# Optimization experiments

Measured on AMD Instinct MI355X. Metric: run time of the kernel, lower is better.

Reference implementation:

```python
import jax, jax.numpy as jnp
import numpy as np

VOCAB, EMBED, HIDDEN, NCLS = 32000, 512, 1024, 1000
BATCH, SEQ = 128, 512


def setup_inputs() -> dict:
    key = jax.random.key(0)
    ks = jax.random.split(key, 8)
    s_in = 1.0 / np.sqrt(EMBED + HIDDEN)
    s_h = 1.0 / np.sqrt(HIDDEN)
    return {
        "x": jax.random.randint(ks[0], (BATCH, SEQ), 0, VOCAB, dtype=jnp.int32),
        "emb": jax.random.normal(ks[1], (VOCAB, EMBED), dtype=jnp.float32),
        "Wz": jax.random.uniform(ks[2], (EMBED + HIDDEN, HIDDEN), jnp.float32, -s_in, s_in),
        "bz": jax.random.uniform(ks[3], (HIDDEN,), jnp.float32, -s_in, s_in),
        "Wh": jax.random.uniform(ks[4], (EMBED + HIDDEN, HIDDEN), jnp.float32, -s_in, s_in),
        "bh": jax.random.uniform(ks[5], (HIDDEN,), jnp.float32, -s_in, s_in),
        "Wfc": jax.random.uniform(ks[6], (HIDDEN, NCLS), jnp.float32, -s_h, s_h),
        "bfc": jax.random.uniform(ks[7], (NCLS,), jnp.float32, -s_h, s_h),
    }


def reference(x, emb, Wz, bz, Wh, bh, Wfc, bfc):
    # embedding lookup: [B, S, E]
    e = emb[x]
    B = x.shape[0]
    h0 = jnp.zeros((B, Wz.shape[1]), dtype=emb.dtype)

    def step(h, x_t):
        c = jnp.concatenate([x_t, h], axis=1)          # [B, E+H]
        z = jax.nn.sigmoid(c @ Wz + bz)                # forget/update gate
        h_tilde = jnp.tanh(c @ Wh + bh)                # candidate state
        h_new = (1.0 - z) * h + z * h_tilde
        return h_new, None

    h_final, _ = jax.lax.scan(step, h0, jnp.swapaxes(e, 0, 1))  # scan over S
    return h_final @ Wfc + bfc                          # logits [B, NCLS]
```

## Files before the change

### kernel.cpp

```cpp
#include <hip/hip_runtime.h>

#define BATCH 128
#define SEQ   512
#define EMB   512
#define HID   1024
#define KC    1536
#define NCLS  1000
#define NBLK  128
#define TPB   512

using short8 = __attribute__((ext_vector_type(8))) short;
using f32x4  = __attribute__((ext_vector_type(4))) float;
typedef unsigned long long u64;

__device__ __forceinline__ short f2bf(float f) {
    unsigned u = __float_as_uint(f);
    unsigned r = (u + 0x7fffu + ((u >> 16) & 1u)) >> 16;
    return (short)r;
}
__device__ __forceinline__ float bf2f(short s) {
    unsigned u = ((unsigned)(unsigned short)s) << 16;
    return __uint_as_float(u);
}

#define OFF_CH0 0u
#define OFF_CL0 262144u
#define OFF_BAR 524288u
#define OFF_CH1 526336u
#define OFF_CL1 788480u
#define OFF_H   1050624u
#define ZERO_I4 32896u

__global__ void mgu_init(int4* __restrict__ ws4) {
    unsigned i = blockIdx.x * blockDim.x + threadIdx.x;
    if (i < ZERO_I4) ws4[i] = make_int4(0, 0, 0, 0);
}

__global__ __launch_bounds__(TPB, 1) void mgu_scan(
    const int* __restrict__ x, const float* __restrict__ emb,
    const float* __restrict__ Wz, const float* __restrict__ bz,
    const float* __restrict__ Wh, const float* __restrict__ bh,
    short* __restrict__ ch0, short* __restrict__ cl0,
    short* __restrict__ ch1, short* __restrict__ cl1,
    unsigned* __restrict__ bars, float* __restrict__ h)
{
    __shared__ short As[16][1544];
    __shared__ short Al[16][1032];

    const int tid  = threadIdx.x;
    const int w    = tid >> 6;
    const int lane = tid & 63;
    const int q    = lane >> 4;
    const int n    = lane & 15;
    const int blk  = blockIdx.x;
    const int r0   = (blk >> 4) << 4;
    const int j0   = (((blk & 15) << 3) + w) << 3;
    unsigned* bar  = bars + ((blk >> 4) << 6);

    const float* Wg = (n < 8) ? Wz : Wh;
    const float* wp = Wg + j0 + (n & 7);
    short8 Bf[48];
#pragma unroll
    for (int ks = 0; ks < 48; ++ks) {
        short8 f;
#pragma unroll
        for (int i = 0; i < 8; ++i)
            f[i] = f2bf(wp[(long)(ks * 32 + q * 8 + i) * HID]);
        Bf[ks] = f;
    }
    const float bzv = bz[j0 + (n & 7)];
    const float bhv = bh[j0 + (n & 7)];

    float hreg[4] = {0.f, 0.f, 0.f, 0.f};

    const int hrow = tid >> 5;
    const int hc0  = (tid & 31) << 4;

    auto stage_emb = [&](int tt) {
        int tok = x[(r0 + hrow) * SEQ + tt];
        const float4* ep = (const float4*)(emb + (long)tok * EMB + hc0);
        float4 e0 = ep[0], e1 = ep[1], e2 = ep[2], e3 = ep[3];
        short8 s0, s1;
        s0[0] = f2bf(e0.x); s0[1] = f2bf(e0.y); s0[2] = f2bf(e0.z); s0[3] = f2bf(e0.w);
        s0[4] = f2bf(e1.x); s0[5] = f2bf(e1.y); s0[6] = f2bf(e1.z); s0[7] = f2bf(e1.w);
        s1[0] = f2bf(e2.x); s1[1] = f2bf(e2.y); s1[2] = f2bf(e2.z); s1[3] = f2bf(e2.w);
        s1[4] = f2bf(e3.x); s1[5] = f2bf(e3.y); s1[6] = f2bf(e3.z); s1[7] = f2bf(e3.w);
        *(short8*)&As[hrow][hc0]     = s0;
        *(short8*)&As[hrow][hc0 + 8] = s1;
    };

    stage_emb(0);

    for (int t = 0; t < SEQ; ++t) {
        const short* chR = (t & 1) ? ch1 : ch0;
        const short* clR = (t & 1) ? cl1 : cl0;
        short*       chW = (t & 1) ? ch0 : ch1;
        short*       clW = (t & 1) ? cl0 : cl1;

        u64 hv[8], lv[8];
#pragma unroll
        for (int k2 = 0; k2 < 8; ++k2) {
            int idx = tid + (k2 << 9);
            int row = idx >> 8;
            int wc  = idx & 255;
            const u64* hp8 = (const u64*)(chR + (r0 + row) * HID);
            const u64* lp8 = (const u64*)(clR + (r0 + row) * HID);
            hv[k2] = __hip_atomic_load(hp8 + wc, __ATOMIC_RELAXED, __HIP_MEMORY_SCOPE_AGENT);
            lv[k2] = __hip_atomic_load(lp8 + wc, __ATOMIC_RELAXED, __HIP_MEMORY_SCOPE_AGENT);
        }
#pragma unroll
        for (int k2 = 0; k2 < 8; ++k2) {
            int idx = tid + (k2 << 9);
            int row = idx >> 8;
            int wc  = idx & 255;
            *(u64*)&As[row][512 + (wc << 2)] = hv[k2];
            *(u64*)&Al[row][wc << 2]         = lv[k2];
        }
        __syncthreads();

        const short* ap  = &As[n][q * 8];
        const short* alp = &Al[n][q * 8];
        f32x4 a0 = {0.f,0.f,0.f,0.f}, a1 = a0, a2 = a0, a3 = a0;
#pragma unroll
        for (int ks = 0; ks < 48; ks += 4) {
            short8 f0 = *(const short8*)(ap + (ks + 0) * 32);
            short8 f1 = *(const short8*)(ap + (ks + 1) * 32);
            short8 f2 = *(const short8*)(ap + (ks + 2) * 32);
            short8 f3 = *(const short8*)(ap + (ks + 3) * 32);
            a0 = __builtin_amdgcn_mfma_f32_16x16x32_bf16(f0, Bf[ks + 0], a0, 0, 0, 0);
            a1 = __builtin_amdgcn_mfma_f32_16x16x32_bf16(f1, Bf[ks + 1], a1, 0, 0, 0);
            a2 = __builtin_amdgcn_mfma_f32_16x16x32_bf16(f2, Bf[ks + 2], a2, 0, 0, 0);
            a3 = __builtin_amdgcn_mfma_f32_16x16x32_bf16(f3, Bf[ks + 3], a3, 0, 0, 0);
        }
#pragma unroll
        for (int e = 0; e < 32; e += 4) {
            short8 g0 = *(const short8*)(alp + (e + 0) * 32);
            short8 g1 = *(const short8*)(alp + (e + 1) * 32);
            short8 g2 = *(const short8*)(alp + (e + 2) * 32);
            short8 g3 = *(const short8*)(alp + (e + 3) * 32);
            a0 = __builtin_amdgcn_mfma_f32_16x16x32_bf16(g0, Bf[16 + e + 0], a0, 0, 0, 0);
            a1 = __builtin_amdgcn_mfma_f32_16x16x32_bf16(g1, Bf[16 + e + 1], a1, 0, 0, 0);
            a2 = __builtin_amdgcn_mfma_f32_16x16x32_bf16(g2, Bf[16 + e + 2], a2, 0, 0, 0);
            a3 = __builtin_amdgcn_mfma_f32_16x16x32_bf16(g3, Bf[16 + e + 3], a3, 0, 0, 0);
        }
        f32x4 acc = (a0 + a1) + (a2 + a3);

        float o0 = __shfl_xor(acc[0], 8, 64);
        float o1 = __shfl_xor(acc[1], 8, 64);
        float o2 = __shfl_xor(acc[2], 8, 64);
        float o3 = __shfl_xor(acc[3], 8, 64);

        if (n < 8) {
            float zp[4] = {acc[0], acc[1], acc[2], acc[3]};
            float tp[4] = {o0, o1, o2, o3};
            const int j = j0 + n;
#pragma unroll
            for (int r2 = 0; r2 < 4; ++r2) {
                float z  = 1.f / (1.f + __expf(-(zp[r2] + bzv)));
                float ht = tanhf(tp[r2] + bhv);
                float ho = hreg[r2];
                float hn = ho + z * (ht - ho);
                hreg[r2] = hn;
                int rr = (r0 + q * 4 + r2) * HID + j;
                if (t < SEQ - 1) {
                    short hi = f2bf(hn);
                    __hip_atomic_store(chW + rr, hi, __ATOMIC_RELAXED, __HIP_MEMORY_SCOPE_AGENT);
                    __hip_atomic_store(clW + rr, f2bf(hn - bf2f(hi)), __ATOMIC_RELAXED, __HIP_MEMORY_SCOPE_AGENT);
                } else {
                    h[rr] = hn;
                }
            }
        }

        if (t < SEQ - 1) {
            __syncthreads();
            if (tid == 0)
                __hip_atomic_fetch_add(bar, 1u, __ATOMIC_RELAXED, __HIP_MEMORY_SCOPE_AGENT);
            stage_emb(t + 1);
            if (tid == 0) {
                unsigned tgt = (unsigned)(t + 1) * 16u;
                while (__hip_atomic_load(bar, __ATOMIC_RELAXED, __HIP_MEMORY_SCOPE_AGENT) < tgt)
                    __builtin_amdgcn_s_sleep(1);
            }
            __syncthreads();
        }
    }
}

__global__ __launch_bounds__(256) void mgu_fc(const float* __restrict__ h,
                                              const float* __restrict__ Wfc,
                                              const float* __restrict__ bfc,
                                              float* __restrict__ out) {
    __shared__ float hs[BATCH][65];
    const int tid = threadIdx.x;
    const int n0  = blockIdx.x * 8;
    const int b   = tid & 127;
    const int nn  = tid >> 7;
    const int nc  = n0 + nn * 4;
    float acc0 = 0.f, acc1 = 0.f, acc2 = 0.f, acc3 = 0.f;

    for (int k0 = 0; k0 < HID; k0 += 64) {
        __syncthreads();
#pragma unroll
        for (int jj = 0; jj < 8; ++jj) {
            int idx = tid + jj * 256;
            int bb  = idx >> 4;
            int kk  = (idx & 15) << 2;
            const float4 v = *(const float4*)(h + bb * HID + k0 + kk);
            hs[bb][kk] = v.x; hs[bb][kk + 1] = v.y; hs[bb][kk + 2] = v.z; hs[bb][kk + 3] = v.w;
        }
        __syncthreads();
#pragma unroll 8
        for (int k = 0; k < 64; ++k) {
            float hv = hs[b][k];
            const float4 wv = *(const float4*)(Wfc + (long)(k0 + k) * NCLS + nc);
            acc0 += hv * wv.x; acc1 += hv * wv.y; acc2 += hv * wv.z; acc3 += hv * wv.w;
        }
    }
    float* op = out + b * NCLS + nc;
    op[0] = acc0 + bfc[nc + 0];
    op[1] = acc1 + bfc[nc + 1];
    op[2] = acc2 + bfc[nc + 2];
    op[3] = acc3 + bfc[nc + 3];
}

extern "C" void kernel_launch(void* const* d_in, const int* in_sizes, int n_in,
                              void* d_out, int out_size, void* d_ws, size_t ws_size,
                              hipStream_t stream) {
    const int*   x   = (const int*)  d_in[0];
    const float* emb = (const float*)d_in[1];
    const float* Wz  = (const float*)d_in[2];
    const float* bz  = (const float*)d_in[3];
    const float* Wh  = (const float*)d_in[4];
    const float* bh  = (const float*)d_in[5];
    const float* Wfc = (const float*)d_in[6];
    const float* bfc = (const float*)d_in[7];
    float* out = (float*)d_out;

    char* ws = (char*)d_ws;
    short*    ch0  = (short*)   (ws + OFF_CH0);
    short*    cl0  = (short*)   (ws + OFF_CL0);
    unsigned* bars = (unsigned*)(ws + OFF_BAR);
    short*    ch1  = (short*)   (ws + OFF_CH1);
    short*    cl1  = (short*)   (ws + OFF_CL1);
    float*    h    = (float*)   (ws + OFF_H);

    mgu_init<<<129, 256, 0, stream>>>((int4*)ws);

    mgu_scan<<<NBLK, TPB, 0, stream>>>(x, emb, Wz, bz, Wh, bh,
                                       ch0, cl0, ch1, cl1, bars, h);

    mgu_fc<<<125, 256, 0, stream>>>(h, Wfc, bfc, out);
}
```

Measured before the change: 3.512 ms.

## Split scan over 256 blocks with per-block flags and fragment-ordered LDS

```diff
diff --git a/kernel.cpp b/kernel.cpp
--- a/kernel.cpp
+++ b/kernel.cpp
@@ -4,14 +4,14 @@
 #define SEQ   512
 #define EMB   512
 #define HID   1024
-#define KC    1536
 #define NCLS  1000
-#define NBLK  128
-#define TPB   512
+#define NBLK  256
+#define TPB   256
 
 using short8 = __attribute__((ext_vector_type(8))) short;
 using f32x4  = __attribute__((ext_vector_type(4))) float;
 typedef unsigned long long u64;
+using u64x2 = __attribute__((ext_vector_type(2))) unsigned long long;
 
 __device__ __forceinline__ short f2bf(float f) {
     unsigned u = __float_as_uint(f);
@@ -24,12 +24,12 @@
 }
 
 #define OFF_CH0 0u
-#define OFF_CL0 262144u
-#define OFF_BAR 524288u
-#define OFF_CH1 526336u
-#define OFF_CL1 788480u
-#define OFF_H   1050624u
-#define ZERO_I4 32896u
+#define OFF_CL0 (256u << 10)
+#define OFF_FLG (512u << 10)
+#define OFF_CH1 (528u << 10)
+#define OFF_CL1 (784u << 10)
+#define OFF_H   (1040u << 10)
+#define ZERO_I4 33792u
 
 __global__ void mgu_init(int4* __restrict__ ws4) {
     unsigned i = blockIdx.x * blockDim.x + threadIdx.x;
@@ -42,10 +42,10 @@
     const float* __restrict__ Wh, const float* __restrict__ bh,
     short* __restrict__ ch0, short* __restrict__ cl0,
     short* __restrict__ ch1, short* __restrict__ cl1,
-    unsigned* __restrict__ bars, float* __restrict__ h)
+    unsigned* __restrict__ flags, float* __restrict__ h)
 {
-    __shared__ short As[16][1544];
-    __shared__ short Al[16][1032];
+    __shared__ short As[48 * 64 * 8];
+    __shared__ short Al[32 * 64 * 8 + 2048];
 
     const int tid  = threadIdx.x;
     const int w    = tid >> 6;
@@ -53,9 +53,10 @@
     const int q    = lane >> 4;
     const int n    = lane & 15;
     const int blk  = blockIdx.x;
-    const int r0   = (blk >> 4) << 4;
-    const int j0   = (((blk & 15) << 3) + w) << 3;
-    unsigned* bar  = bars + ((blk >> 4) << 6);
+    const int rg   = blk >> 5;
+    const int r0   = rg << 4;
+    const int pb   = blk & 31;
+    const int j0   = (((blk & 31) << 2) + w) << 3;
 
     const float* Wg = (n < 8) ? Wz : Wh;
     const float* wp = Wg + j0 + (n & 7);
@@ -73,20 +74,19 @@
 
     float hreg[4] = {0.f, 0.f, 0.f, 0.f};
 
-    const int hrow = tid >> 5;
-    const int hc0  = (tid & 31) << 4;
-
     auto stage_emb = [&](int tt) {
-        int tok = x[(r0 + hrow) * SEQ + tt];
-        const float4* ep = (const float4*)(emb + (long)tok * EMB + hc0);
-        float4 e0 = ep[0], e1 = ep[1], e2 = ep[2], e3 = ep[3];
-        short8 s0, s1;
-        s0[0] = f2bf(e0.x); s0[1] = f2bf(e0.y); s0[2] = f2bf(e0.z); s0[3] = f2bf(e0.w);
-        s0[4] = f2bf(e1.x); s0[5] = f2bf(e1.y); s0[6] = f2bf(e1.z); s0[7] = f2bf(e1.w);
-        s1[0] = f2bf(e2.x); s1[1] = f2bf(e2.y); s1[2] = f2bf(e2.z); s1[3] = f2bf(e2.w);
-        s1[4] = f2bf(e3.x); s1[5] = f2bf(e3.y); s1[6] = f2bf(e3.z); s1[7] = f2bf(e3.w);
-        *(short8*)&As[hrow][hc0]     = s0;
-        *(short8*)&As[hrow][hc0 + 8] = s1;
+#pragma unroll
+        for (int i = 0; i < 4; ++i) {
+            int s  = tid + (i << 8);
+            int nn = s & 15, qq = (s >> 4) & 3, ks = s >> 6;
+            int tok = x[(r0 + nn) * SEQ + tt];
+            const float4* ep = (const float4*)(emb + (long)tok * EMB + ks * 32 + qq * 8);
+            float4 e0 = ep[0], e1 = ep[1];
+            short8 v;
+            v[0] = f2bf(e0.x); v[1] = f2bf(e0.y); v[2] = f2bf(e0.z); v[3] = f2bf(e0.w);
+            v[4] = f2bf(e1.x); v[5] = f2bf(e1.y); v[6] = f2bf(e1.z); v[7] = f2bf(e1.w);
+            *(short8*)&As[s * 8] = v;
+        }
     };
 
     stage_emb(0);
@@ -97,36 +97,57 @@
         short*       chW = (t & 1) ? ch0 : ch1;
         short*       clW = (t & 1) ? cl0 : cl1;
 
-        u64 hv[8], lv[8];
-#pragma unroll
-        for (int k2 = 0; k2 < 8; ++k2) {
-            int idx = tid + (k2 << 9);
-            int row = idx >> 8;
-            int wc  = idx & 255;
-            const u64* hp8 = (const u64*)(chR + (r0 + row) * HID);
-            const u64* lp8 = (const u64*)(clR + (r0 + row) * HID);
-            hv[k2] = __hip_atomic_load(hp8 + wc, __ATOMIC_RELAXED, __HIP_MEMORY_SCOPE_AGENT);
-            lv[k2] = __hip_atomic_load(lp8 + wc, __ATOMIC_RELAXED, __HIP_MEMORY_SCOPE_AGENT);
-        }
-#pragma unroll
-        for (int k2 = 0; k2 < 8; ++k2) {
-            int idx = tid + (k2 << 9);
-            int row = idx >> 8;
-            int wc  = idx & 255;
-            *(u64*)&As[row][512 + (wc << 2)] = hv[k2];
-            *(u64*)&Al[row][wc << 2]         = lv[k2];
-        }
-        __syncthreads();
-
-        const short* ap  = &As[n][q * 8];
-        const short* alp = &Al[n][q * 8];
+        if (t > 0 && w == 0) {
+            const unsigned* fp = flags + (((rg << 5) + (lane & 31)) << 4);
+            const unsigned tgt = (unsigned)t;
+            for (;;) {
+                unsigned f = __hip_atomic_load(fp, __ATOMIC_RELAXED, __HIP_MEMORY_SCOPE_AGENT);
+                if (!__ballot((lane < 32) && (f < tgt))) break;
+                __builtin_amdgcn_s_sleep(1);
+            }
+        }
+        __syncthreads();
+
+        u64 hv[16], lv[16];
+#pragma unroll
+        for (int i = 0; i < 8; ++i) {
+            int s  = 1024 + tid + (i << 8);
+            int nn = s & 15, qq = (s >> 4) & 3, ks = s >> 6;
+            const u64* gp = (const u64*)(chR + (r0 + nn) * HID + (ks * 32 + qq * 8 - 512));
+            hv[2 * i]     = __hip_atomic_load(gp,     __ATOMIC_RELAXED, __HIP_MEMORY_SCOPE_AGENT);
+            hv[2 * i + 1] = __hip_atomic_load(gp + 1, __ATOMIC_RELAXED, __HIP_MEMORY_SCOPE_AGENT);
+        }
+#pragma unroll
+        for (int i = 0; i < 8; ++i) {
+            int s  = tid + (i << 8);
+            int nn = s & 15, qq = (s >> 4) & 3, ks = s >> 6;
+            const u64* gp = (const u64*)(clR + (r0 + nn) * HID + (ks * 32 + qq * 8));
+            lv[2 * i]     = __hip_atomic_load(gp,     __ATOMIC_RELAXED, __HIP_MEMORY_SCOPE_AGENT);
+            lv[2 * i + 1] = __hip_atomic_load(gp + 1, __ATOMIC_RELAXED, __HIP_MEMORY_SCOPE_AGENT);
+        }
+#pragma unroll
+        for (int i = 0; i < 8; ++i) {
+            int s = 1024 + tid + (i << 8);
+            u64x2 v; v[0] = hv[2 * i]; v[1] = hv[2 * i + 1];
+            *(u64x2*)&As[s * 8] = v;
+        }
+#pragma unroll
+        for (int i = 0; i < 8; ++i) {
+            int s = tid + (i << 8);
+            u64x2 v; v[0] = lv[2 * i]; v[1] = lv[2 * i + 1];
+            *(u64x2*)&Al[s * 8] = v;
+        }
+        __syncthreads();
+
+        const short* ap  = &As[lane * 8];
+        const short* alp = &Al[lane * 8];
         f32x4 a0 = {0.f,0.f,0.f,0.f}, a1 = a0, a2 = a0, a3 = a0;
 #pragma unroll
         for (int ks = 0; ks < 48; ks += 4) {
-            short8 f0 = *(const short8*)(ap + (ks + 0) * 32);
-            short8 f1 = *(const short8*)(ap + (ks + 1) * 32);
-            short8 f2 = *(const short8*)(ap + (ks + 2) * 32);
-            short8 f3 = *(const short8*)(ap + (ks + 3) * 32);
+            short8 f0 = *(const short8*)(ap + (ks + 0) * 512);
+            short8 f1 = *(const short8*)(ap + (ks + 1) * 512);
+            short8 f2 = *(const short8*)(ap + (ks + 2) * 512);
+            short8 f3 = *(const short8*)(ap + (ks + 3) * 512);
             a0 = __builtin_amdgcn_mfma_f32_16x16x32_bf16(f0, Bf[ks + 0], a0, 0, 0, 0);
             a1 = __builtin_amdgcn_mfma_f32_16x16x32_bf16(f1, Bf[ks + 1], a1, 0, 0, 0);
             a2 = __builtin_amdgcn_mfma_f32_16x16x32_bf16(f2, Bf[ks + 2], a2, 0, 0, 0);
@@ -134,10 +155,10 @@
         }
 #pragma unroll
         for (int e = 0; e < 32; e += 4) {
-            short8 g0 = *(const short8*)(alp + (e + 0) * 32);
-            short8 g1 = *(const short8*)(alp + (e + 1) * 32);
-            short8 g2 = *(const short8*)(alp + (e + 2) * 32);
-            short8 g3 = *(const short8*)(alp + (e + 3) * 32);
+            short8 g0 = *(const short8*)(alp + (e + 0) * 512);
+            short8 g1 = *(const short8*)(alp + (e + 1) * 512);
+            short8 g2 = *(const short8*)(alp + (e + 2) * 512);
+            short8 g3 = *(const short8*)(alp + (e + 3) * 512);
             a0 = __builtin_amdgcn_mfma_f32_16x16x32_bf16(g0, Bf[16 + e + 0], a0, 0, 0, 0);
             a1 = __builtin_amdgcn_mfma_f32_16x16x32_bf16(g1, Bf[16 + e + 1], a1, 0, 0, 0);
             a2 = __builtin_amdgcn_mfma_f32_16x16x32_bf16(g2, Bf[16 + e + 2], a2, 0, 0, 0);
@@ -175,14 +196,9 @@
         if (t < SEQ - 1) {
             __syncthreads();
             if (tid == 0)
-                __hip_atomic_fetch_add(bar, 1u, __ATOMIC_RELAXED, __HIP_MEMORY_SCOPE_AGENT);
+                __hip_atomic_store(flags + (((rg << 5) + pb) << 4), (unsigned)(t + 1),
+                                   __ATOMIC_RELAXED, __HIP_MEMORY_SCOPE_AGENT);
             stage_emb(t + 1);
-            if (tid == 0) {
-                unsigned tgt = (unsigned)(t + 1) * 16u;
-                while (__hip_atomic_load(bar, __ATOMIC_RELAXED, __HIP_MEMORY_SCOPE_AGENT) < tgt)
-                    __builtin_amdgcn_s_sleep(1);
-            }
-            __syncthreads();
         }
     }
 }
@@ -238,17 +254,17 @@
     float* out = (float*)d_out;
 
     char* ws = (char*)d_ws;
-    short*    ch0  = (short*)   (ws + OFF_CH0);
-    short*    cl0  = (short*)   (ws + OFF_CL0);
-    unsigned* bars = (unsigned*)(ws + OFF_BAR);
-    short*    ch1  = (short*)   (ws + OFF_CH1);
-    short*    cl1  = (short*)   (ws + OFF_CL1);
-    float*    h    = (float*)   (ws + OFF_H);
-
-    mgu_init<<<129, 256, 0, stream>>>((int4*)ws);
+    short*    ch0   = (short*)   (ws + OFF_CH0);
+    short*    cl0   = (short*)   (ws + OFF_CL0);
+    unsigned* flags = (unsigned*)(ws + OFF_FLG);
+    short*    ch1   = (short*)   (ws + OFF_CH1);
+    short*    cl1   = (short*)   (ws + OFF_CL1);
+    float*    h     = (float*)   (ws + OFF_H);
+
+    mgu_init<<<132, 256, 0, stream>>>((int4*)ws);
 
     mgu_scan<<<NBLK, TPB, 0, stream>>>(x, emb, Wz, bz, Wh, bh,
-                                       ch0, cl0, ch1, cl1, bars, h);
+                                       ch0, cl0, ch1, cl1, flags, h);
 
     mgu_fc<<<125, 256, 0, stream>>>(h, Wfc, bfc, out);
 }
```

New measurement: 4.549 ms. 1.3x slower.
